# Optimization experiments

Hardware: AMD Instinct MI355X
Metric: run time of the kernel (lower is better)

The kernel has to match this reference:

```python
import jax, jax.numpy as jnp
import numpy as np
import itertools, string

# Weight space: 2-layer MLP params, flattened in dict-key order (W1, W2, b1, b2).
SPECS = [(0, 1), (1, 2), (1,), (2,)]
N = 1024            # size of each permutable dim (perm ids 0,1,2)
C_IN, C_OUT = 16, 16
NUM_TERMS = [9, 10, 7, 6]   # equivariant basis terms per output leaf


def _set_partitions(elems):
    if not elems:
        yield []
        return
    first, rest = elems[0], elems[1:]
    for part in _set_partitions(rest):
        for i in range(len(part)):
            yield part[:i] + [part[i] + [first]] + part[i + 1:]
        yield part + [[first]]


def gen_basis(out_spec, in_spec, out_dims, x):
    """All permutation-equivariant basis maps from x (*in_dims, c) to (*out_dims, c).
    Basis elements <-> set partitions of (in,out) axis positions sharing a perm id:
    in-axes in a block are diagonalized; in-only blocks are summed; mixed blocks copy
    the axis to the matching out position; out-only blocks broadcast."""
    pos = ([('in', a, p) for a, p in enumerate(in_spec)]
           + [('out', a, p) for a, p in enumerate(out_spec)])
    by_pid = {}
    for q in pos:
        by_pid.setdefault(q[2], []).append(q)
    parts = [list(_set_partitions(by_pid[p])) for p in sorted(by_pid)]
    terms = []
    for combo in itertools.product(*parts):
        blocks = [b for part in combo for b in part]
        pos2b = {(q[0], q[1]): bi for bi, b in enumerate(blocks) for q in b}
        L = string.ascii_lowercase
        in_sub = ''.join(L[pos2b[('in', a)]] for a in range(len(in_spec)))
        mixed = [bi for bi, b in enumerate(blocks)
                 if any(q[0] == 'in' for q in b) and any(q[0] == 'out' for q in b)]
        out_sub = ''.join(L[bi] for bi in mixed)
        # diagonal over repeated in-axes, sum over in-only blocks; z = channel axis
        t = jnp.einsum(f'{in_sub}z->{out_sub}z', x)
        targets = [min(q[1] for q in blocks[bi] if q[0] == 'out') for bi in mixed]
        t = jnp.transpose(t, list(np.argsort(targets)) + [len(mixed)])
        st = sorted(targets)
        for ax in range(len(out_dims)):
            if ax not in st:
                t = jnp.expand_dims(t, ax)
        t = jnp.broadcast_to(t, tuple(out_dims) + (x.shape[-1],))
        for b in blocks:  # diagonal-embed blocks with >1 out axis (not hit for MLP specs)
            outs = sorted(q[1] for q in b if q[0] == 'out')
            for a1, a2 in zip(outs, outs[1:]):
                n = out_dims[a1]
                sh = [1] * (len(out_dims) + 1)
                sh[a1] = n; sh[a2] = n
                t = t * jnp.eye(n, dtype=x.dtype).reshape(sh)
        terms.append(t)
    return terms


def _forward(flat, thetas, biases):
    outs = []
    for i in range(len(flat)):
        out_dims = flat[i].shape[:-1]
        acc = jnp.zeros(tuple(out_dims) + (C_OUT,), dtype=flat[i].dtype)
        k = 0
        for j in range(len(flat)):
            for term in gen_basis(SPECS[i], SPECS[j], out_dims, flat[j]):
                acc = acc + jnp.einsum('...i,io->...o', term, thetas[i][k])
                k += 1
        outs.append(acc + biases[i])
    return tuple(outs)


def setup_inputs() -> dict:
    key = jax.random.key(0)
    ks = jax.random.split(key, 12)
    inp = {
        'W1': jax.random.normal(ks[0], (N, N, C_IN), jnp.float32),
        'W2': jax.random.normal(ks[1], (N, N, C_IN), jnp.float32),
        'b1': jax.random.normal(ks[2], (N, C_IN), jnp.float32),
        'b2': jax.random.normal(ks[3], (N, C_IN), jnp.float32),
    }
    for i, k in enumerate(NUM_TERMS):
        scale = (1.0 / (C_IN * k)) ** 0.5
        inp[f'theta_{i}'] = scale * jax.random.normal(ks[4 + i], (k, C_IN, C_OUT), jnp.float32)
        inp[f'bias_{i}'] = jnp.zeros((C_OUT,), jnp.float32)
    return inp


def reference(W1, W2, b1, b2, theta_0, theta_1, theta_2, theta_3,
              bias_0, bias_1, bias_2, bias_3):
    return _forward([W1, W2, b1, b2],
                    [theta_0, theta_1, theta_2, theta_3],
                    [bias_0, bias_1, bias_2, bias_3])
```

## Files before the change

kernel.cpp:

```cpp
#include <hip/hip_runtime.h>

#define NDIM 1024
#define CH 16
#define ROW_FLOATS (NDIM * CH)
#define ROW_F4 (ROW_FLOATS / 4)

__device__ inline float4 f4add(float4 a, float4 b) {
    return make_float4(a.x + b.x, a.y + b.y, a.z + b.z, a.w + b.w);
}
__device__ inline float4 f4shfl_xor(float4 v, int m) {
    return make_float4(__shfl_xor(v.x, m), __shfl_xor(v.y, m),
                       __shfl_xor(v.z, m), __shfl_xor(v.w, m));
}

__global__ __launch_bounds__(256) void k_fused(const float* __restrict__ W1,
                                               const float* __restrict__ W2,
                                               float* __restrict__ rowpart,
                                               float* __restrict__ colpart) {
    int t  = threadIdx.x;
    int bj = blockIdx.x, bi = blockIdx.y, z = blockIdx.z;
    int j0 = bj * 64, i0 = bi * 64;
    const float4* base = (const float4*)(z ? W2 : W1)
                       + (size_t)i0 * ROW_F4 + j0 * 4 + t;
    __shared__ float rowacc[4][64][16];
    int w = t >> 6, lane = t & 63;
    float4 colacc = make_float4(0.f, 0.f, 0.f, 0.f);
#pragma unroll 4
    for (int k = 0; k < 64; ++k) {
        float4 v = base[(size_t)k * ROW_F4];
        colacc = f4add(colacc, v);
        float4 vr = v;
        vr = f4add(vr, f4shfl_xor(vr, 4));
        vr = f4add(vr, f4shfl_xor(vr, 8));
        vr = f4add(vr, f4shfl_xor(vr, 16));
        vr = f4add(vr, f4shfl_xor(vr, 32));
        if (lane < 4) {
            rowacc[w][k][lane * 4 + 0] = vr.x;
            rowacc[w][k][lane * 4 + 1] = vr.y;
            rowacc[w][k][lane * 4 + 2] = vr.z;
            rowacc[w][k][lane * 4 + 3] = vr.w;
        }
    }
    int jl = t >> 2, cq = t & 3;
    {
        size_t coff = (((size_t)z * 16 + bi) * NDIM + (j0 + jl)) * CH + cq * 4;
        *(float4*)(colpart + coff) = colacc;
    }
    __syncthreads();
    {
        int r = t >> 2;
        const float4* ra = (const float4*)&rowacc[0][0][0];
        float4 s = f4add(f4add(ra[(0 * 64 + r) * 4 + cq], ra[(1 * 64 + r) * 4 + cq]),
                         f4add(ra[(2 * 64 + r) * 4 + cq], ra[(3 * 64 + r) * 4 + cq]));
        size_t roff = (((size_t)z * 16 + bj) * NDIM + (i0 + r)) * CH + cq * 4;
        *(float4*)(rowpart + roff) = s;
    }
}

__global__ __launch_bounds__(256) void k_finalize(const float* __restrict__ rowpart,
                                                  const float* __restrict__ colpart,
                                                  float* __restrict__ rowsumF,
                                                  float* __restrict__ colsumF) {
    int gt  = blockIdx.x * 256 + threadIdx.x;
    int sel = gt >> 15;
    int rem = gt & 32767;
    const float* src = sel ? colpart : rowpart;
    float* dst       = sel ? colsumF : rowsumF;
    int z = rem >> 14, idx = rem & 16383;
    const float* p = src + (size_t)z * 16 * 16384 + idx;
    float s = 0.f;
#pragma unroll
    for (int ch = 0; ch < 16; ++ch) s += p[ch * 16384];
    dst[rem] = s;
}

__global__ __launch_bounds__(256) void k_sums(const float* __restrict__ rowsum,
                                              const float* __restrict__ b1,
                                              const float* __restrict__ b2,
                                              float* __restrict__ sums) {
    int tgt = blockIdx.x;
    const float* src = (tgt == 0) ? rowsum
                     : (tgt == 1) ? rowsum + 16384
                     : (tgt == 2) ? b1 : b2;
    int t = threadIdx.x;
    const float4* s4 = (const float4*)src;
    float4 a = make_float4(0.f, 0.f, 0.f, 0.f);
#pragma unroll
    for (int k = 0; k < 16; ++k) a = f4add(a, s4[t + 256 * k]);
    __shared__ float4 lds[256];
    lds[t] = a;
    __syncthreads();
    if (t < 64) {
        float4 s = lds[t];
#pragma unroll
        for (int o = 1; o < 4; ++o) s = f4add(s, lds[t + 64 * o]);
        lds[t] = s;
    }
    __syncthreads();
    if (t < 4) {
        float4 s = make_float4(0.f, 0.f, 0.f, 0.f);
#pragma unroll
        for (int m = 0; m < 16; ++m) s = f4add(s, lds[t + 4 * m]);
        float* dst = sums + tgt * 16 + 4 * t;
        dst[0] = s.x; dst[1] = s.y; dst[2] = s.z; dst[3] = s.w;
    }
}

__global__ __launch_bounds__(256) void k_smalls(const float* __restrict__ rowsum,
                                                const float* __restrict__ colsum,
                                                const float* __restrict__ sums,
                                                const float* __restrict__ b1,
                                                const float* __restrict__ b2,
                                                const float* __restrict__ th0,
                                                const float* __restrict__ th1,
                                                const float* __restrict__ th2,
                                                const float* __restrict__ th3,
                                                const float* __restrict__ bias0,
                                                const float* __restrict__ bias1,
                                                const float* __restrict__ bias2,
                                                const float* __restrict__ bias3,
                                                float* __restrict__ R0, float* __restrict__ C0,
                                                float* __restrict__ R1, float* __restrict__ C1,
                                                float* __restrict__ out2, float* __restrict__ out3) {
    int gt = blockIdx.x * 256 + threadIdx.x;
    int i = gt >> 4, o = gt & 15;
    const float* rs1 = rowsum + i * 16;
    const float* rs2 = rowsum + 16384 + i * 16;
    const float* cs1 = colsum + i * 16;
    const float* cs2 = colsum + 16384 + i * 16;
    const float* b1i = b1 + i * 16;
    const float* b2i = b2 + i * 16;
    float r0 = 0.f, c0a = 0.f, r1 = 0.f, c1a = 0.f, o2 = 0.f, o3 = 0.f;
    float k0 = 0.f, k1 = 0.f, k2 = 0.f, k3 = 0.f;
#pragma unroll
    for (int c = 0; c < 16; ++c) {
        float sW1 = sums[c], sW2 = sums[16 + c], sb1 = sums[32 + c], sb2 = sums[48 + c];
        r0  += rs1[c] * th0[(1 * 16 + c) * 16 + o];
        c0a += cs1[c] * th0[(2 * 16 + c) * 16 + o]
             + rs2[c] * th0[(4 * 16 + c) * 16 + o]
             + b1i[c] * th0[(6 * 16 + c) * 16 + o];
        k0  += sW1 * th0[(3 * 16 + c) * 16 + o] + sW2 * th0[(5 * 16 + c) * 16 + o]
             + sb1 * th0[(7 * 16 + c) * 16 + o] + sb2 * th0[(8 * 16 + c) * 16 + o];
        r1  += cs1[c] * th1[(0 * 16 + c) * 16 + o]
             + rs2[c] * th1[(3 * 16 + c) * 16 + o]
             + b1i[c] * th1[(6 * 16 + c) * 16 + o];
        c1a += cs2[c] * th1[(4 * 16 + c) * 16 + o]
             + b2i[c] * th1[(8 * 16 + c) * 16 + o];
        k1  += sW1 * th1[(1 * 16 + c) * 16 + o] + sW2 * th1[(5 * 16 + c) * 16 + o]
             + sb1 * th1[(7 * 16 + c) * 16 + o] + sb2 * th1[(9 * 16 + c) * 16 + o];
        o2  += cs1[c] * th2[(0 * 16 + c) * 16 + o]
             + rs2[c] * th2[(2 * 16 + c) * 16 + o]
             + b1i[c] * th2[(4 * 16 + c) * 16 + o];
        k2  += sW1 * th2[(1 * 16 + c) * 16 + o] + sW2 * th2[(3 * 16 + c) * 16 + o]
             + sb1 * th2[(5 * 16 + c) * 16 + o] + sb2 * th2[(6 * 16 + c) * 16 + o];
        o3  += cs2[c] * th3[(1 * 16 + c) * 16 + o]
             + b2i[c] * th3[(4 * 16 + c) * 16 + o];
        k3  += sW1 * th3[(0 * 16 + c) * 16 + o] + sW2 * th3[(2 * 16 + c) * 16 + o]
             + sb1 * th3[(3 * 16 + c) * 16 + o] + sb2 * th3[(5 * 16 + c) * 16 + o];
    }
    R0[gt]   = r0;
    C0[gt]   = c0a + k0 + bias0[o];
    R1[gt]   = r1;
    C1[gt]   = c1a + k1 + bias1[o];
    out2[gt] = o2 + k2 + bias2[o];
    out3[gt] = o3 + k3 + bias3[o];
}

__global__ __launch_bounds__(256) void k_main(const float* __restrict__ W1,
                                              const float* __restrict__ W2,
                                              const float* __restrict__ R0,
                                              const float* __restrict__ C0,
                                              const float* __restrict__ R1,
                                              const float* __restrict__ C1,
                                              const float* __restrict__ th0,
                                              const float* __restrict__ th1,
                                              float* __restrict__ out0,
                                              float* __restrict__ out1) {
    int z = blockIdx.z;
    const float* W  = z ? W2 : W1;
    const float* R  = z ? R1 : R0;
    const float* Cc = z ? C1 : C0;
    const float* TH = z ? th1 : th0;
    float* out      = z ? out1 : out0;

    int t = threadIdx.x;
    int i = blockIdx.y;
    int j = blockIdx.x * 256 + t;

    __shared__ float th[256];
    __shared__ float r[16];
    th[t] = TH[t];
    if (t < 16) r[t] = R[i * 16 + t];
    __syncthreads();

    size_t base = ((size_t)i * NDIM + j) * CH;
    const float4* xp = (const float4*)(W + base);
    float4 x0 = xp[0], x1 = xp[1], x2 = xp[2], x3 = xp[3];
    float x[16] = {x0.x, x0.y, x0.z, x0.w, x1.x, x1.y, x1.z, x1.w,
                   x2.x, x2.y, x2.z, x2.w, x3.x, x3.y, x3.z, x3.w};

    const float4* cj = (const float4*)(Cc + j * 16);
    float4 c0 = cj[0], c1 = cj[1], c2 = cj[2], c3 = cj[3];
    float acc[16] = {c0.x, c0.y, c0.z, c0.w, c1.x, c1.y, c1.z, c1.w,
                     c2.x, c2.y, c2.z, c2.w, c3.x, c3.y, c3.z, c3.w};
#pragma unroll
    for (int o = 0; o < 16; ++o) acc[o] += r[o];
#pragma unroll
    for (int c = 0; c < 16; ++c) {
        float xv = x[c];
#pragma unroll
        for (int o = 0; o < 16; ++o) acc[o] += xv * th[c * 16 + o];
    }
    float4* op = (float4*)(out + base);
    op[0] = make_float4(acc[0],  acc[1],  acc[2],  acc[3]);
    op[1] = make_float4(acc[4],  acc[5],  acc[6],  acc[7]);
    op[2] = make_float4(acc[8],  acc[9],  acc[10], acc[11]);
    op[3] = make_float4(acc[12], acc[13], acc[14], acc[15]);
}

extern "C" void kernel_launch(void* const* d_in, const int* in_sizes, int n_in,
                              void* d_out, int out_size, void* d_ws, size_t ws_size,
                              hipStream_t stream) {
    const float* W1    = (const float*)d_in[0];
    const float* W2    = (const float*)d_in[1];
    const float* b1    = (const float*)d_in[2];
    const float* b2    = (const float*)d_in[3];
    const float* th0   = (const float*)d_in[4];
    const float* bias0 = (const float*)d_in[5];
    const float* th1   = (const float*)d_in[6];
    const float* bias1 = (const float*)d_in[7];
    const float* th2   = (const float*)d_in[8];
    const float* bias2 = (const float*)d_in[9];
    const float* th3   = (const float*)d_in[10];
    const float* bias3 = (const float*)d_in[11];

    float* out  = (float*)d_out;
    float* out0 = out;
    float* out1 = out + (size_t)NDIM * NDIM * CH;
    float* out2 = out1 + (size_t)NDIM * NDIM * CH;
    float* out3 = out2 + (size_t)NDIM * CH;

    float* rowpart = out0;
    float* colpart = out0 + 524288;

    float* ws      = (float*)d_ws;
    float* rowsumF = ws;
    float* colsumF = ws + 32768;
    float* sums    = ws + 65536;
    float* R0      = ws + 65600;
    float* C0      = R0 + 16384;
    float* R1      = C0 + 16384;
    float* C1      = R1 + 16384;

    k_fused<<<dim3(16, 16, 2), dim3(256), 0, stream>>>(W1, W2, rowpart, colpart);
    k_finalize<<<dim3(256), dim3(256), 0, stream>>>(rowpart, colpart, rowsumF, colsumF);
    k_sums<<<dim3(4), dim3(256), 0, stream>>>(rowsumF, b1, b2, sums);
    k_smalls<<<dim3(64), dim3(256), 0, stream>>>(rowsumF, colsumF, sums, b1, b2,
                                                 th0, th1, th2, th3,
                                                 bias0, bias1, bias2, bias3,
                                                 R0, C0, R1, C1, out2, out3);
    k_main<<<dim3(4, NDIM, 2), dim3(256), 0, stream>>>(W1, W2, R0, C0, R1, C1,
                                                       th0, th1 + 2 * 256,
                                                       out0, out1);
}
```

Baseline: 104.1 us.

## Retile row/col reduction kernel to 16-row tiles with LDS-staged row sums

The fused reduction kernel now processes 16x64 tiles instead of 64x64, launching four times as many blocks. Row sums are computed by staging the tile in padded shared memory and having 64 threads sum across it, replacing the per-iteration wave shuffles. Column partials grow from 16 to 64 slices per matrix, so the finalize kernel sums more partials for the column half. The aim is more parallelism and less shuffle overhead in the kernel that reads both full weight matrices, at the cost of more partial traffic and a serial 64-step LDS reduction done by only one wave.

```diff
diff --git a/kernel.cpp b/kernel.cpp
--- a/kernel.cpp
+++ b/kernel.cpp
@@ -7,10 +7,6 @@
 
 __device__ inline float4 f4add(float4 a, float4 b) {
     return make_float4(a.x + b.x, a.y + b.y, a.z + b.z, a.w + b.w);
-}
-__device__ inline float4 f4shfl_xor(float4 v, int m) {
-    return make_float4(__shfl_xor(v.x, m), __shfl_xor(v.y, m),
-                       __shfl_xor(v.z, m), __shfl_xor(v.w, m));
 }
 
 __global__ __launch_bounds__(256) void k_fused(const float* __restrict__ W1,
@@ -18,42 +14,27 @@
                                                float* __restrict__ rowpart,
                                                float* __restrict__ colpart) {
     int t  = threadIdx.x;
-    int bj = blockIdx.x, bi = blockIdx.y, z = blockIdx.z;
-    int j0 = bj * 64, i0 = bi * 64;
-    const float4* base = (const float4*)(z ? W2 : W1)
-                       + (size_t)i0 * ROW_F4 + j0 * 4 + t;
-    __shared__ float rowacc[4][64][16];
-    int w = t >> 6, lane = t & 63;
+    int jt = blockIdx.x, it = blockIdx.y, z = blockIdx.z;
+    int i0 = it * 16, j0 = jt * 64;
+    const float4* Wf4 = (const float4*)(z ? W2 : W1);
+    const float4* base = Wf4 + (size_t)i0 * ROW_F4 + jt * 256 + t;
+
+    __shared__ float4 tile[16][257];
     float4 colacc = make_float4(0.f, 0.f, 0.f, 0.f);
-#pragma unroll 4
-    for (int k = 0; k < 64; ++k) {
-        float4 v = base[(size_t)k * ROW_F4];
+#pragma unroll
+    for (int r = 0; r < 16; ++r) {
+        float4 v = base[(size_t)r * ROW_F4];
         colacc = f4add(colacc, v);
-        float4 vr = v;
-        vr = f4add(vr, f4shfl_xor(vr, 4));
-        vr = f4add(vr, f4shfl_xor(vr, 8));
-        vr = f4add(vr, f4shfl_xor(vr, 16));
-        vr = f4add(vr, f4shfl_xor(vr, 32));
-        if (lane < 4) {
-            rowacc[w][k][lane * 4 + 0] = vr.x;
-            rowacc[w][k][lane * 4 + 1] = vr.y;
-            rowacc[w][k][lane * 4 + 2] = vr.z;
-            rowacc[w][k][lane * 4 + 3] = vr.w;
-        }
-    }
-    int jl = t >> 2, cq = t & 3;
-    {
-        size_t coff = (((size_t)z * 16 + bi) * NDIM + (j0 + jl)) * CH + cq * 4;
-        *(float4*)(colpart + coff) = colacc;
-    }
-    __syncthreads();
-    {
-        int r = t >> 2;
-        const float4* ra = (const float4*)&rowacc[0][0][0];
-        float4 s = f4add(f4add(ra[(0 * 64 + r) * 4 + cq], ra[(1 * 64 + r) * 4 + cq]),
-                         f4add(ra[(2 * 64 + r) * 4 + cq], ra[(3 * 64 + r) * 4 + cq]));
-        size_t roff = (((size_t)z * 16 + bj) * NDIM + (i0 + r)) * CH + cq * 4;
-        *(float4*)(rowpart + roff) = s;
+        tile[r][t] = v;
+    }
+    ((float4*)colpart)[(((size_t)z * 64 + it) * NDIM + j0) * 4 + t] = colacc;
+    __syncthreads();
+    if (t < 64) {
+        int r = t >> 2, cq = t & 3;
+        float4 s = make_float4(0.f, 0.f, 0.f, 0.f);
+#pragma unroll
+        for (int jl = 0; jl < 64; ++jl) s = f4add(s, tile[r][jl * 4 + cq]);
+        ((float4*)rowpart)[(((size_t)z * 16 + jt) * NDIM + (i0 + r)) * 4 + cq] = s;
     }
 }
 
@@ -61,17 +42,23 @@
                                                   const float* __restrict__ colpart,
                                                   float* __restrict__ rowsumF,
                                                   float* __restrict__ colsumF) {
-    int gt  = blockIdx.x * 256 + threadIdx.x;
-    int sel = gt >> 15;
-    int rem = gt & 32767;
-    const float* src = sel ? colpart : rowpart;
-    float* dst       = sel ? colsumF : rowsumF;
-    int z = rem >> 14, idx = rem & 16383;
-    const float* p = src + (size_t)z * 16 * 16384 + idx;
-    float s = 0.f;
-#pragma unroll
-    for (int ch = 0; ch < 16; ++ch) s += p[ch * 16384];
-    dst[rem] = s;
+    int gt = blockIdx.x * 256 + threadIdx.x;
+    if (gt < 32768) {
+        int z = gt >> 14, idx = gt & 16383;
+        const float* p = rowpart + (size_t)z * 16 * 16384 + idx;
+        float s = 0.f;
+#pragma unroll
+        for (int c = 0; c < 16; ++c) s += p[(size_t)c * 16384];
+        rowsumF[gt] = s;
+    } else {
+        int rem = gt - 32768;
+        int z = rem >> 14, idx = rem & 16383;
+        const float* p = colpart + (size_t)z * 64 * 16384 + idx;
+        float s = 0.f;
+#pragma unroll
+        for (int c = 0; c < 64; ++c) s += p[(size_t)c * 16384];
+        colsumF[rem] = s;
+    }
 }
 
 __global__ __launch_bounds__(256) void k_sums(const float* __restrict__ rowsum,
@@ -252,7 +239,7 @@
     float* R1      = C0 + 16384;
     float* C1      = R1 + 16384;
 
-    k_fused<<<dim3(16, 16, 2), dim3(256), 0, stream>>>(W1, W2, rowpart, colpart);
+    k_fused<<<dim3(16, 64, 2), dim3(256), 0, stream>>>(W1, W2, rowpart, colpart);
     k_finalize<<<dim3(256), dim3(256), 0, stream>>>(rowpart, colpart, rowsumF, colsumF);
     k_sums<<<dim3(4), dim3(256), 0, stream>>>(rowsumF, b1, b2, sums);
     k_smalls<<<dim3(64), dim3(256), 0, stream>>>(rowsumF, colsumF, sums, b1, b2,
```

New measurement: 105.5 us. Within noise of the previous version (+1.3%).
